# Kernel tuning notes

Measured on AMD Instinct MI355X. Metric: run time of the kernel, lower is better.

Reference implementation:

```python
import jax, jax.numpy as jnp
import numpy as np

B, N, E = 8, 1024, 10
ITERS = 3


def setup_inputs() -> dict:
    key = jax.random.key(0)
    ks = jax.random.split(key, 17)

    def lin(kw, kb, out_d, in_d):
        # xavier-normal-ish weights, small random bias (torch Linear has bias)
        w = jax.random.normal(kw, (out_d, in_d), jnp.float32) * np.float32(np.sqrt(2.0 / (in_d + out_d)))
        b = jax.random.normal(kb, (out_d,), jnp.float32) * np.float32(0.01)
        return w, b

    sel_w, sel_b = lin(ks[0], ks[1], E, 1)        # w_selected: Linear(1, E)
    nbp_w, nbp_b = lin(ks[2], ks[3], E, E)        # w_nbpriors: Linear(E, E)
    nbw_w, nbw_b = lin(ks[4], ks[5], E, E)        # w_nbweights: Linear(E, E)
    nbwew_w, nbwew_b = lin(ks[6], ks[7], E, 1)    # w_nbweights_ew: Linear(1, E)
    qred_w, qred_b = lin(ks[8], ks[9], 1, 2 * E)  # w_q_reduc: Linear(2E, 1)
    qall_w, qall_b = lin(ks[10], ks[11], E, E)    # w_q_allembed: Linear(E, E)
    qact_w, qact_b = lin(ks[12], ks[13], E, E)    # w_q_action: Linear(E, E)

    features = jax.random.normal(ks[14], (B, N), jnp.float32)
    weights = jax.random.uniform(ks[15], (B, N, N), jnp.float32)
    adjacency = jax.random.uniform(ks[16], (B, N, N), jnp.float32)

    return dict(features=features, weights=weights, adjacency=adjacency,
                sel_w=sel_w, sel_b=sel_b, nbp_w=nbp_w, nbp_b=nbp_b,
                nbw_w=nbw_w, nbw_b=nbw_b, nbwew_w=nbwew_w, nbwew_b=nbwew_b,
                qred_w=qred_w, qred_b=qred_b, qall_w=qall_w, qall_b=qall_b,
                qact_w=qact_w, qact_b=qact_b)


def reference(features, weights, adjacency,
              sel_w, sel_b, nbp_w, nbp_b, nbw_w, nbw_b,
              nbwew_w, nbwew_b, qred_w, qred_b,
              qall_w, qall_b, qact_w, qact_b):
    b, n = features.shape
    e = sel_w.shape[0]

    # v_selected = Linear(1,E)(features[...,None]) -> [B, N, E]
    v_selected = features[:, :, None] * sel_w[:, 0] + sel_b

    # edge-weight embedding: relu(Linear(1,E)(weights[...,None])) -> [B, N, N, E]
    we = jax.nn.relu(weights[..., None] * nbwew_w[:, 0] + nbwew_b)
    # sum over source-node dim (dim=1), then Linear(E,E) -> [B, N, E]
    v_weights = jnp.einsum('bne,oe->bno', we.sum(axis=1), nbw_w) + nbw_b

    base = v_selected + v_weights
    emb = jnp.zeros((b, n, e), features.dtype)
    for _ in range(ITERS):
        v_priors = jnp.einsum('bij,bje->bie', adjacency, emb)
        v_priors = jnp.einsum('bie,oe->bio', v_priors, nbp_w) + nbp_b
        emb = jax.nn.relu(base + v_priors)

    # global readout -> broadcast per node
    sumembed = jnp.einsum('be,oe->bo', emb.sum(axis=1), qall_w) + qall_b   # [B, E]
    peract = jnp.einsum('bne,oe->bno', emb, qact_w) + qact_b               # [B, N, E]
    cat = jnp.concatenate(
        [jnp.broadcast_to(sumembed[:, None, :], peract.shape), peract], axis=-1)  # [B, N, 2E]
    q_vals = (jnp.einsum('bnf,of->bno', cat, qred_w) + qred_b)[:, :, 0]    # [B, N]
    return q_vals, emb
```

## Files before the change

kernel.cpp:

```cpp
#include <hip/hip_runtime.h>

#define E10 10

__global__ __launch_bounds__(256) void k_wsum(const float* __restrict__ W,
                                              const float* __restrict__ eww,
                                              const float* __restrict__ ewb,
                                              float* __restrict__ Spart) {
    const int t  = threadIdx.x;
    const int jt = blockIdx.x;
    const int ic = blockIdx.y;
    const int b  = blockIdx.z;
    const int cp = t & 15;
    const int rg = t >> 4;
    const int j0 = jt * 32 + cp * 2;
    const int i0 = ic * 128 + rg * 8;

    float cw[E10], cb[E10];
#pragma unroll
    for (int e = 0; e < E10; e++) { cw[e] = eww[e]; cb[e] = ewb[e]; }

    float a0[E10], a1[E10];
#pragma unroll
    for (int e = 0; e < E10; e++) { a0[e] = 0.f; a1[e] = 0.f; }

    const float* Wp = W + ((size_t)(b * 1024 + i0) << 10) + j0;
#pragma unroll
    for (int r = 0; r < 8; r++) {
        const float2 w = *(const float2*)(Wp + ((size_t)r << 10));
#pragma unroll
        for (int e = 0; e < E10; e++) {
            a0[e] += fmaxf(w.x * cw[e] + cb[e], 0.f);
            a1[e] += fmaxf(w.y * cw[e] + cb[e], 0.f);
        }
    }

    __shared__ float smf[16][32][E10];
#pragma unroll
    for (int e = 0; e < E10; e++) {
        smf[rg][cp * 2][e]     = a0[e];
        smf[rg][cp * 2 + 1][e] = a1[e];
    }
    __syncthreads();
    if (t < 32) {
        float S[E10];
#pragma unroll
        for (int e = 0; e < E10; e++) S[e] = smf[0][t][e];
#pragma unroll
        for (int r = 1; r < 16; r++)
#pragma unroll
            for (int e = 0; e < E10; e++) S[e] += smf[r][t][e];
        float2* Sp = (float2*)(Spart + ((size_t)(ic * 8192 + b * 1024 + jt * 32 + t)) * E10);
#pragma unroll
        for (int q = 0; q < 5; q++) Sp[q] = make_float2(S[2 * q], S[2 * q + 1]);
    }
}

__global__ __launch_bounds__(256) void k_base(const float* __restrict__ Spart,
                                              const float* __restrict__ feat,
                                              const float* __restrict__ selw,
                                              const float* __restrict__ selb,
                                              const float* __restrict__ nbww,
                                              const float* __restrict__ nbwb,
                                              const float* __restrict__ nbpb,
                                              float* __restrict__ base,
                                              float* __restrict__ embA) {
    const int t = threadIdx.x;
    const int g = t & 31;
    const int m = t >> 5;
    const int node = blockIdx.x * 32 + g;

    float S[E10];
    const float2* p = (const float2*)(Spart + ((size_t)(m * 8192 + node)) * E10);
#pragma unroll
    for (int q = 0; q < 5; q++) {
        const float2 v = p[q];
        S[2 * q] = v.x;
        S[2 * q + 1] = v.y;
    }

    __shared__ float lds[8][32][E10];
#pragma unroll
    for (int e = 0; e < E10; e++) lds[m][g][e] = S[e];
    __syncthreads();
    if (m == 0) {
#pragma unroll
        for (int mm = 1; mm < 8; mm++)
#pragma unroll
            for (int e = 0; e < E10; e++) S[e] += lds[mm][g][e];
        const float f = feat[node];
#pragma unroll
        for (int o = 0; o < E10; o++) {
            float vw = nbwb[o];
#pragma unroll
            for (int e = 0; e < E10; e++) vw += S[e] * nbww[o * E10 + e];
            const float bv = f * selw[o] + selb[o] + vw;
            base[(size_t)node * E10 + o] = bv;
            embA[(size_t)node * E10 + o] = fmaxf(bv + nbpb[o], 0.f);
        }
    }
}

__global__ __launch_bounds__(256) void k_iter(const float* __restrict__ A,
                                              const float* __restrict__ embIn,
                                              const float* __restrict__ base,
                                              const float* __restrict__ nbpw,
                                              const float* __restrict__ nbpb,
                                              float* __restrict__ embOut) {
    __shared__ __align__(16) float2 l2[5 * 1024];
    const int t    = threadIdx.x;
    const int b    = blockIdx.y;
    const int lane = t & 63;
    const int wave = t >> 6;
    const int lg   = lane >> 4;
    const int ll   = lane & 15;

    const float2* src = (const float2*)(embIn + (size_t)b * 10240);
    for (int jj = t; jj < 1024; jj += 256) {
#pragma unroll
        for (int e2 = 0; e2 < 5; e2++) l2[e2 * 1024 + jj] = src[jj * 5 + e2];
    }

    const int o = (ll < E10) ? ll : 0;
    float nw[E10];
    const float pb = nbpb[o];
#pragma unroll
    for (int e = 0; e < E10; e++) nw[e] = nbpw[o * E10 + e];
    __syncthreads();

    const int rowA = blockIdx.x * 32 + wave * 8 + lg * 2;
    const float* ArA = A + (((size_t)b << 10) + rowA << 10);
    const float* ArB = ArA + 1024;

    float accA[E10], accB[E10];
#pragma unroll
    for (int e = 0; e < E10; e++) { accA[e] = 0.f; accB[e] = 0.f; }

    float4 a4A = *(const float4*)(ArA + ll * 4);
    float4 a4B = *(const float4*)(ArB + ll * 4);
#pragma unroll
    for (int k = 0; k < 16; k++) {
        const int j0 = ll * 4 + k * 64;
        float4 nA, nB;
        if (k < 15) {
            nA = *(const float4*)(ArA + j0 + 64);
            nB = *(const float4*)(ArB + j0 + 64);
        }
#pragma unroll
        for (int e2 = 0; e2 < 5; e2++) {
            const float4* lp = (const float4*)&l2[e2 * 1024 + j0];
            const float4 qa = lp[0];
            const float4 qb = lp[1];
            accA[2 * e2]     += a4A.x * qa.x + a4A.y * qa.z + a4A.z * qb.x + a4A.w * qb.z;
            accA[2 * e2 + 1] += a4A.x * qa.y + a4A.y * qa.w + a4A.z * qb.y + a4A.w * qb.w;
            accB[2 * e2]     += a4B.x * qa.x + a4B.y * qa.z + a4B.z * qb.x + a4B.w * qb.z;
            accB[2 * e2 + 1] += a4B.x * qa.y + a4B.y * qa.w + a4B.z * qb.y + a4B.w * qb.w;
        }
        if (k < 15) { a4A = nA; a4B = nB; }
    }

#pragma unroll
    for (int e = 0; e < E10; e++) {
        float v = accA[e];
        v += __shfl_xor(v, 8);
        v += __shfl_xor(v, 4);
        v += __shfl_xor(v, 2);
        v += __shfl_xor(v, 1);
        accA[e] = v;
        float w = accB[e];
        w += __shfl_xor(w, 8);
        w += __shfl_xor(w, 4);
        w += __shfl_xor(w, 2);
        w += __shfl_xor(w, 1);
        accB[e] = w;
    }

    if (ll < E10) {
        float pA = pb, pB = pb;
#pragma unroll
        for (int e = 0; e < E10; e++) {
            pA += accA[e] * nw[e];
            pB += accB[e] * nw[e];
        }
        const size_t offA = ((size_t)b * 1024 + rowA) * E10 + o;
        embOut[offA]       = fmaxf(base[offA] + pA, 0.f);
        embOut[offA + E10] = fmaxf(base[offA + E10] + pB, 0.f);
    }
}

__global__ __launch_bounds__(256) void k_final(const float* __restrict__ emb,
                                               const float* __restrict__ qallw,
                                               const float* __restrict__ qallb,
                                               const float* __restrict__ qredw,
                                               const float* __restrict__ qredb,
                                               const float* __restrict__ qactw,
                                               const float* __restrict__ qactb,
                                               float* __restrict__ out) {
    const int t = threadIdx.x;
    const int b = blockIdx.x >> 2;
    const int qt = blockIdx.x & 3;
    const int lane = t & 63, wave = t >> 6;

    float S[E10];
#pragma unroll
    for (int e = 0; e < E10; e++) S[e] = 0.f;
    for (int n = t; n < 1024; n += 256) {
        const float2* p = (const float2*)(emb + ((size_t)b * 1024 + n) * E10);
#pragma unroll
        for (int q = 0; q < 5; q++) {
            const float2 v = p[q];
            S[2 * q] += v.x;
            S[2 * q + 1] += v.y;
        }
    }
#pragma unroll
    for (int e = 0; e < E10; e++) {
        float v = S[e];
        v += __shfl_xor(v, 32);
        v += __shfl_xor(v, 16);
        v += __shfl_xor(v, 8);
        v += __shfl_xor(v, 4);
        v += __shfl_xor(v, 2);
        v += __shfl_xor(v, 1);
        S[e] = v;
    }
    __shared__ float lds[4][E10];
    __shared__ float sdot_s;
    if (lane == 0) {
#pragma unroll
        for (int e = 0; e < E10; e++) lds[wave][e] = S[e];
    }
    __syncthreads();
    if (t == 0) {
        float Sf[E10];
#pragma unroll
        for (int e = 0; e < E10; e++)
            Sf[e] = lds[0][e] + lds[1][e] + lds[2][e] + lds[3][e];
        float sd = 0.f;
#pragma unroll
        for (int o = 0; o < E10; o++) {
            float se = qallb[o];
#pragma unroll
            for (int e = 0; e < E10; e++) se += Sf[e] * qallw[o * E10 + e];
            sd += se * qredw[o];
        }
        sdot_s = sd;
    }
    __syncthreads();

    const int node = b * 1024 + qt * 256 + t;
    float v[E10];
    const float2* p = (const float2*)(emb + (size_t)node * E10);
#pragma unroll
    for (int q = 0; q < 5; q++) {
        const float2 w = p[q];
        v[2 * q] = w.x;
        v[2 * q + 1] = w.y;
    }
    float qv = qredb[0] + sdot_s;
#pragma unroll
    for (int o = 0; o < E10; o++) {
        float pa = qactb[o];
#pragma unroll
        for (int e = 0; e < E10; e++) pa += v[e] * qactw[o * E10 + e];
        qv += pa * qredw[E10 + o];
    }
    out[node] = qv;
    float2* o2 = (float2*)(out + 8192 + (size_t)node * E10);
#pragma unroll
    for (int q = 0; q < 5; q++) o2[q] = make_float2(v[2 * q], v[2 * q + 1]);
}

extern "C" void kernel_launch(void* const* d_in, const int* in_sizes, int n_in,
                              void* d_out, int out_size, void* d_ws, size_t ws_size,
                              hipStream_t stream) {
    (void)in_sizes; (void)n_in; (void)out_size; (void)ws_size;
    const float* features  = (const float*)d_in[0];
    const float* weights   = (const float*)d_in[1];
    const float* adjacency = (const float*)d_in[2];
    const float* sel_w     = (const float*)d_in[3];
    const float* sel_b     = (const float*)d_in[4];
    const float* nbp_w     = (const float*)d_in[5];
    const float* nbp_b     = (const float*)d_in[6];
    const float* nbw_w     = (const float*)d_in[7];
    const float* nbw_b     = (const float*)d_in[8];
    const float* nbwew_w   = (const float*)d_in[9];
    const float* nbwew_b   = (const float*)d_in[10];
    const float* qred_w    = (const float*)d_in[11];
    const float* qred_b    = (const float*)d_in[12];
    const float* qall_w    = (const float*)d_in[13];
    const float* qall_b    = (const float*)d_in[14];
    const float* qact_w    = (const float*)d_in[15];
    const float* qact_b    = (const float*)d_in[16];
    float* out = (float*)d_out;
    float* ws  = (float*)d_ws;

    float* Spart = ws;
    float* base  = ws + 655360;
    float* embA  = base + 81920;
    float* embB  = embA + 81920;

    k_wsum<<<dim3(32, 8, 8), 256, 0, stream>>>(weights, nbwew_w, nbwew_b, Spart);
    k_base<<<256, 256, 0, stream>>>(Spart, features, sel_w, sel_b, nbw_w, nbw_b, nbp_b,
                                    base, embA);
    k_iter<<<dim3(32, 8), 256, 0, stream>>>(adjacency, embA, base, nbp_w, nbp_b, embB);
    k_iter<<<dim3(32, 8), 256, 0, stream>>>(adjacency, embB, base, nbp_w, nbp_b, embA);
    k_final<<<32, 256, 0, stream>>>(embA, qall_w, qall_b, qred_w, qred_b,
                                    qact_w, qact_b, out);
}
```

Baseline: 44.82 us.

## Remap k_iter to 16 rows per block with full-wave row reduction

The adjacency-times-embedding kernel now gives each wave 4 rows. All 64 lanes stride across a row with float2 loads, and a full 64-lane shuffle reduction replaces the old 16-lane split where each lane held 2 rows. The grid doubles to 64 row-chunks per batch, which gives more blocks for occupancy. The LDS staging loop is rewritten to read the source contiguously. In exchange, each block re-stages the whole 40KB embedding into LDS for half as many rows, and the shuffle reductions roughly triple.

Result: slower. 62.75 us (+40.0%).

```diff
diff --git a/kernel.cpp b/kernel.cpp
--- a/kernel.cpp
+++ b/kernel.cpp
@@ -100,24 +100,23 @@
     }
 }
 
-__global__ __launch_bounds__(256) void k_iter(const float* __restrict__ A,
-                                              const float* __restrict__ embIn,
-                                              const float* __restrict__ base,
-                                              const float* __restrict__ nbpw,
-                                              const float* __restrict__ nbpb,
-                                              float* __restrict__ embOut) {
+__global__ __launch_bounds__(256) void k_iter(
+    const float* __restrict__ A,
+    const float* __restrict__ embIn,
+    const float* __restrict__ base,
+    const float* __restrict__ nbpw, const float* __restrict__ nbpb,
+    float* __restrict__ embOut)
+{
     __shared__ __align__(16) float2 l2[5 * 1024];
-    const int t    = threadIdx.x;
-    const int b    = blockIdx.y;
-    const int lane = t & 63;
-    const int wave = t >> 6;
-    const int lg   = lane >> 4;
-    const int ll   = lane & 15;
+    const int t = threadIdx.x;
+    const int rc = blockIdx.x, b = blockIdx.y;
+    const int lane = t & 63, wv = t >> 6;
+    const int lg = lane >> 4, ll = lane & 15;
 
     const float2* src = (const float2*)(embIn + (size_t)b * 10240);
-    for (int jj = t; jj < 1024; jj += 256) {
-#pragma unroll
-        for (int e2 = 0; e2 < 5; e2++) l2[e2 * 1024 + jj] = src[jj * 5 + e2];
+    for (int idx = t; idx < 5120; idx += 256) {
+        const int j = idx / 5, e2 = idx - j * 5;
+        l2[e2 * 1024 + j] = src[idx];
     }
 
     const int o = (ll < E10) ? ll : 0;
@@ -127,64 +126,79 @@
     for (int e = 0; e < E10; e++) nw[e] = nbpw[o * E10 + e];
     __syncthreads();
 
-    const int rowA = blockIdx.x * 32 + wave * 8 + lg * 2;
-    const float* ArA = A + (((size_t)b << 10) + rowA << 10);
-    const float* ArB = ArA + 1024;
-
-    float accA[E10], accB[E10];
-#pragma unroll
-    for (int e = 0; e < E10; e++) { accA[e] = 0.f; accB[e] = 0.f; }
-
-    float4 a4A = *(const float4*)(ArA + ll * 4);
-    float4 a4B = *(const float4*)(ArB + ll * 4);
-#pragma unroll
-    for (int k = 0; k < 16; k++) {
-        const int j0 = ll * 4 + k * 64;
-        float4 nA, nB;
-        if (k < 15) {
-            nA = *(const float4*)(ArA + j0 + 64);
-            nB = *(const float4*)(ArB + j0 + 64);
-        }
-#pragma unroll
-        for (int e2 = 0; e2 < 5; e2++) {
-            const float4* lp = (const float4*)&l2[e2 * 1024 + j0];
-            const float4 qa = lp[0];
-            const float4 qb = lp[1];
-            accA[2 * e2]     += a4A.x * qa.x + a4A.y * qa.z + a4A.z * qb.x + a4A.w * qb.z;
-            accA[2 * e2 + 1] += a4A.x * qa.y + a4A.y * qa.w + a4A.z * qb.y + a4A.w * qb.w;
-            accB[2 * e2]     += a4B.x * qa.x + a4B.y * qa.z + a4B.z * qb.x + a4B.w * qb.z;
-            accB[2 * e2 + 1] += a4B.x * qa.y + a4B.y * qa.w + a4B.z * qb.y + a4B.w * qb.w;
-        }
-        if (k < 15) { a4A = nA; a4B = nB; }
-    }
-
-#pragma unroll
-    for (int e = 0; e < E10; e++) {
-        float v = accA[e];
-        v += __shfl_xor(v, 8);
-        v += __shfl_xor(v, 4);
-        v += __shfl_xor(v, 2);
-        v += __shfl_xor(v, 1);
-        accA[e] = v;
-        float w = accB[e];
-        w += __shfl_xor(w, 8);
-        w += __shfl_xor(w, 4);
-        w += __shfl_xor(w, 2);
-        w += __shfl_xor(w, 1);
-        accB[e] = w;
-    }
-
-    if (ll < E10) {
-        float pA = pb, pB = pb;
+    const int row0 = rc * 16 + wv * 4;
+    const float* Ab = A + (((size_t)(b * 1024 + row0)) << 10);
+
+    float acc[4][E10];
+#pragma unroll
+    for (int r = 0; r < 4; r++)
+#pragma unroll
+        for (int e = 0; e < E10; e++) acc[r][e] = 0.f;
+
+    const float4* L4 = (const float4*)l2;
+
+    float2 cur[4], nxt[4];
+#pragma unroll
+    for (int r = 0; r < 4; r++)
+        cur[r] = *(const float2*)(Ab + ((size_t)r << 10) + lane * 2);
+#pragma unroll
+    for (int k = 0; k < 8; k++) {
+        if (k < 7) {
+#pragma unroll
+            for (int r = 0; r < 4; r++)
+                nxt[r] = *(const float2*)(Ab + ((size_t)r << 10) + lane * 2 + (k + 1) * 128);
+        }
+        const int q0 = lane + k * 64;
+        const float4 p0 = L4[q0];
+        const float4 p1 = L4[512 + q0];
+        const float4 p2 = L4[1024 + q0];
+        const float4 p3 = L4[1536 + q0];
+        const float4 p4 = L4[2048 + q0];
+#pragma unroll
+        for (int r = 0; r < 4; r++) {
+            const float2 a = cur[r];
+            acc[r][0] += a.x * p0.x + a.y * p0.z;
+            acc[r][1] += a.x * p0.y + a.y * p0.w;
+            acc[r][2] += a.x * p1.x + a.y * p1.z;
+            acc[r][3] += a.x * p1.y + a.y * p1.w;
+            acc[r][4] += a.x * p2.x + a.y * p2.z;
+            acc[r][5] += a.x * p2.y + a.y * p2.w;
+            acc[r][6] += a.x * p3.x + a.y * p3.z;
+            acc[r][7] += a.x * p3.y + a.y * p3.w;
+            acc[r][8] += a.x * p4.x + a.y * p4.z;
+            acc[r][9] += a.x * p4.y + a.y * p4.w;
+        }
+#pragma unroll
+        for (int r = 0; r < 4; r++) cur[r] = nxt[r];
+    }
+
+#pragma unroll
+    for (int r = 0; r < 4; r++)
 #pragma unroll
         for (int e = 0; e < E10; e++) {
-            pA += accA[e] * nw[e];
-            pB += accB[e] * nw[e];
-        }
-        const size_t offA = ((size_t)b * 1024 + rowA) * E10 + o;
-        embOut[offA]       = fmaxf(base[offA] + pA, 0.f);
-        embOut[offA + E10] = fmaxf(base[offA + E10] + pB, 0.f);
-    }
+            float v = acc[r][e];
+            v += __shfl_xor(v, 32);
+            v += __shfl_xor(v, 16);
+            v += __shfl_xor(v, 8);
+            v += __shfl_xor(v, 4);
+            v += __shfl_xor(v, 2);
+            v += __shfl_xor(v, 1);
+            acc[r][e] = v;
+        }
+
+    float te[E10];
+#pragma unroll
+    for (int e = 0; e < E10; e++)
+        te[e] = (lg == 0) ? acc[0][e] : (lg == 1) ? acc[1][e]
+              : (lg == 2) ? acc[2][e] : acc[3][e];
+
+    float p = pb;
+#pragma unroll
+    for (int e = 0; e < E10; e++) p += te[e] * nw[e];
+
+    const int row = row0 + lg;
+    const size_t off = ((size_t)(b * 1024 + row)) * E10 + o;
+    if (ll < E10) embOut[off] = fmaxf(base[off] + p, 0.f);
 }
 
 __global__ __launch_bounds__(256) void k_final(const float* __restrict__ emb,
@@ -300,10 +314,10 @@
     float* embB  = embA + 81920;
 
     k_wsum<<<dim3(32, 8, 8), 256, 0, stream>>>(weights, nbwew_w, nbwew_b, Spart);
-    k_base<<<256, 256, 0, stream>>>(Spart, features, sel_w, sel_b, nbw_w, nbw_b, nbp_b,
-                                    base, embA);
-    k_iter<<<dim3(32, 8), 256, 0, stream>>>(adjacency, embA, base, nbp_w, nbp_b, embB);
-    k_iter<<<dim3(32, 8), 256, 0, stream>>>(adjacency, embB, base, nbp_w, nbp_b, embA);
+    k_base<<<256, 256, 0, stream>>>(Spart, features, sel_w, sel_b, nbw_w, nbw_b,
+                                    nbp_b, base, embA);
+    k_iter<<<dim3(64, 8), 256, 0, stream>>>(adjacency, embA, base, nbp_w, nbp_b, embB);
+    k_iter<<<dim3(64, 8), 256, 0, stream>>>(adjacency, embB, base, nbp_w, nbp_b, embA);
     k_final<<<32, 256, 0, stream>>>(embA, qall_w, qall_b, qred_w, qred_b,
                                     qact_w, qact_b, out);
 }
```
